# Performance work log

Hardware: AMD Instinct MI355X
Metric: run time of the kernel (lower is better)

Reference implementation:

```python
import jax, jax.numpy as jnp
import numpy as np

D_QK = 32  # out_channels // 8


def conv1x1(x, w, b):
    # x: [B,C,H,W], w: [O,C], b: [O] -> [B,O,H,W]
    return jnp.einsum('bchw,oc->bohw', x, w) + b[None, :, None, None]


def setup_inputs() -> dict:
    key = jax.random.key(0)
    ks = jax.random.split(key, 10)
    B, C, H, W = 4, 256, 64, 64
    in_ch, out_ch, attn_ch = 512, 256, 256
    s_in = 1.0 / np.sqrt(in_ch)
    s_at = 1.0 / np.sqrt(attn_ch)
    return {
        'ef': jax.random.normal(ks[0], (B, C, H, W), jnp.float32),
        'sf': jax.random.normal(ks[1], (B, C, H, W), jnp.float32),
        'Attn': jax.random.normal(ks[2], (B, attn_ch, H, W), jnp.float32),
        'Qw': jax.random.uniform(ks[3], (D_QK, in_ch), jnp.float32, -s_in, s_in),
        'Qb': jax.random.uniform(ks[4], (D_QK,), jnp.float32, -s_in, s_in),
        'Kw': jax.random.uniform(ks[5], (D_QK, attn_ch), jnp.float32, -s_at, s_at),
        'Kb': jax.random.uniform(ks[6], (D_QK,), jnp.float32, -s_at, s_at),
        'Vw': jax.random.uniform(ks[7], (out_ch, in_ch), jnp.float32, -s_in, s_in),
        'Vb': jax.random.uniform(ks[8], (out_ch,), jnp.float32, -s_in, s_in),
        'gamma': jnp.ones((1,), jnp.float32) * 0.25,
    }


def reference(ef, sf, Attn, Qw, Qb, Kw, Kb, Vw, Vb, gamma):
    B, C, H, W = ef.shape
    N = H * W
    x = jnp.concatenate((ef, sf), axis=1)  # [B, 2C, H, W]
    q = conv1x1(x, Qw, Qb).reshape(B, D_QK, N)         # [B, d, N]
    k = conv1x1(Attn, Kw, Kb).reshape(B, D_QK, N)      # [B, d, N]
    # scores[b, m, n] = sum_d q[b, d, m] * k[b, d, n]  (no 1/sqrt(d) scale)
    scores = jnp.einsum('bdm,bdn->bmn', q, k)
    attn = jax.nn.softmax(scores, axis=-1)             # [B, N, N]
    v = conv1x1(x, Vw, Vb).reshape(B, C, N)            # [B, C, N]
    # out[b, c, m] = sum_n v[b, c, n] * attn[b, m, n]
    out = jnp.einsum('bcn,bmn->bcm', v, attn).reshape(B, C, H, W)
    return gamma[0] * out + ef
```

## Files before the change

kernel.cpp:

```cpp
#include <hip/hip_runtime.h>
#include <hip/hip_bf16.h>

typedef short bf16x8 __attribute__((ext_vector_type(8)));
typedef float f32x4 __attribute__((ext_vector_type(4)));

#define MFMA16(a, b, c) __builtin_amdgcn_mfma_f32_16x16x32_bf16(a, b, c, 0, 0, 0)

#define NB 4
#define NC 256
#define NSP 4096
#define LOG2E 1.4426950408889634f

__device__ __forceinline__ unsigned short f2bf(float f) {
    return (unsigned short)((__float_as_uint(f) + 0x8000u) >> 16);
}
__device__ __forceinline__ unsigned pk2bf(float hi, float lo) {
    return __builtin_amdgcn_perm(__float_as_uint(hi) + 0x8000u,
                                 __float_as_uint(lo) + 0x8000u, 0x07060302u);
}

__global__ __launch_bounds__(256) void prep_w(
    const float* __restrict__ Qw, const float* __restrict__ Kw,
    const float* __restrict__ Vw,
    unsigned short* __restrict__ Qwbf, unsigned short* __restrict__ Kwbf,
    unsigned short* __restrict__ Vwbf)
{
    int i = blockIdx.x * 256 + threadIdx.x;
    {
        const float4* vs = (const float4*)(Vw + (size_t)i * 8);
        float4 a = vs[0], c = vs[1];
        int4 st;
        st.x = (int)pk2bf(a.y, a.x); st.y = (int)pk2bf(a.w, a.z);
        st.z = (int)pk2bf(c.y, c.x); st.w = (int)pk2bf(c.w, c.z);
        *(int4*)(Vwbf + (size_t)i * 8) = st;
    }
    if (i < 2048) {
        const float4* qs = (const float4*)(Qw + (size_t)i * 8);
        float4 a = qs[0], c = qs[1];
        int4 st;
        st.x = (int)pk2bf(a.y, a.x); st.y = (int)pk2bf(a.w, a.z);
        st.z = (int)pk2bf(c.y, c.x); st.w = (int)pk2bf(c.w, c.z);
        *(int4*)(Qwbf + (size_t)i * 8) = st;
    }
    if (i < 1024) {
        const float4* ks = (const float4*)(Kw + (size_t)i * 8);
        float4 a = ks[0], c = ks[1];
        int4 st;
        st.x = (int)pk2bf(a.y, a.x); st.y = (int)pk2bf(a.w, a.z);
        st.z = (int)pk2bf(c.y, c.x); st.w = (int)pk2bf(c.w, c.z);
        *(int4*)(Kwbf + (size_t)i * 8) = st;
    }
}

__global__ __launch_bounds__(256) void proj_qv(
    const float* __restrict__ ef, const float* __restrict__ sf,
    const unsigned short* __restrict__ Qwbf, const float* __restrict__ Qb,
    const unsigned short* __restrict__ Vwbf, const float* __restrict__ Vb,
    unsigned short* __restrict__ qws, unsigned short* __restrict__ vws)
{
    __shared__ __align__(16) unsigned short xt[32][72];

    int t = threadIdx.x;
    int w = t >> 6, lane = t & 63, quad = lane >> 4, l15 = lane & 15;
    int mt = blockIdx.x, b = blockIdx.y, m0 = mt * 32;
    int ci = t & 63, sm = t >> 6;
    int mi = w >> 1, oh = w & 1;

    f32x4 zero = {0.f, 0.f, 0.f, 0.f};
    f32x4 acc[2][4];
#pragma unroll
    for (int m = 0; m < 2; ++m)
#pragma unroll
        for (int ot = 0; ot < 4; ++ot) acc[m][ot] = zero;
    f32x4 qacc = zero;

    const float* s0p = ef + ((size_t)(b * NC) + ci) * NSP + m0 + sm * 8;
    float4 x0 = *(const float4*)s0p;
    float4 x1 = *(const float4*)(s0p + 4);

    for (int c = 0; c < 8; ++c) {
        float4 n0 = x0, n1 = x1;
        if (c < 7) {
            int cn = c + 1;
            const float* sn = (cn < 4 ? ef : sf) +
                              ((size_t)(b * NC) + (cn & 3) * 64 + ci) * NSP + m0 + sm * 8;
            n0 = *(const float4*)sn;
            n1 = *(const float4*)(sn + 4);
        }
        __syncthreads();
        unsigned short* xd = &xt[sm * 8][ci];
        xd[0]   = f2bf(x0.x); xd[72]  = f2bf(x0.y);
        xd[144] = f2bf(x0.z); xd[216] = f2bf(x0.w);
        xd[288] = f2bf(x1.x); xd[360] = f2bf(x1.y);
        xd[432] = f2bf(x1.z); xd[504] = f2bf(x1.w);
        __syncthreads();
        int ci0 = c * 64;
#pragma unroll
        for (int ks = 0; ks < 2; ++ks) {
            bf16x8 a0 = *(const bf16x8*)&xt[l15][ks * 32 + quad * 8];
            bf16x8 a1 = *(const bf16x8*)&xt[16 + l15][ks * 32 + quad * 8];
            bf16x8 bq = *(const bf16x8*)(Qwbf + (size_t)(oh * 16 + l15) * 512 + ci0 + ks * 32 + quad * 8);
            qacc = MFMA16(mi ? a1 : a0, bq, qacc);
#pragma unroll
            for (int ot = 0; ot < 4; ++ot) {
                bf16x8 bv = *(const bf16x8*)(Vwbf + (size_t)(w * 64 + ot * 16 + l15) * 512 + ci0 + ks * 32 + quad * 8);
                acc[0][ot] = MFMA16(a0, bv, acc[0][ot]);
                acc[1][ot] = MFMA16(a1, bv, acc[1][ot]);
            }
        }
        x0 = n0; x1 = n1;
    }

#pragma unroll
    for (int ot = 0; ot < 4; ++ot) {
        int ch = w * 64 + ot * 16 + l15;
        float bias = Vb[ch];
        unsigned* vp = (unsigned*)(vws + ((size_t)((b * 128 + mt) * 256 + ch)) * 32);
#pragma unroll
        for (int r = 0; r < 4; ++r)
            vp[quad * 4 + r] = pk2bf(acc[1][ot][r] + bias, acc[0][ot][r] + bias);
    }

    {
        int o = oh * 16 + l15;
        float bb = Qb[o];
#pragma unroll
        for (int r = 0; r < 4; ++r) {
            int m = m0 + mi * 16 + quad * 4 + r;
            qws[((size_t)(b * NSP) + m) * 32 + o] = f2bf((qacc[r] + bb) * LOG2E);
        }
    }
}

__global__ __launch_bounds__(256) void proj_k(
    const float* __restrict__ attn,
    const unsigned short* __restrict__ Kwbf, const float* __restrict__ Kb,
    unsigned short* __restrict__ kws)
{
    __shared__ __align__(16) unsigned short xt[32][72];

    int t = threadIdx.x;
    int w = t >> 6, lane = t & 63, quad = lane >> 4, l15 = lane & 15;
    int mt = blockIdx.x, b = blockIdx.y, m0 = mt * 32;
    int ci = t & 63, sm = t >> 6;
    int mi = w >> 1, oh = w & 1;

    f32x4 acc = {0.f, 0.f, 0.f, 0.f};

    const float* s0p = attn + ((size_t)(b * NC) + ci) * NSP + m0 + sm * 8;
    float4 x0 = *(const float4*)s0p;
    float4 x1 = *(const float4*)(s0p + 4);

    for (int c = 0; c < 4; ++c) {
        float4 n0 = x0, n1 = x1;
        if (c < 3) {
            const float* sn = attn + ((size_t)(b * NC) + (c + 1) * 64 + ci) * NSP + m0 + sm * 8;
            n0 = *(const float4*)sn;
            n1 = *(const float4*)(sn + 4);
        }
        __syncthreads();
        unsigned short* xd = &xt[sm * 8][ci];
        xd[0]   = f2bf(x0.x); xd[72]  = f2bf(x0.y);
        xd[144] = f2bf(x0.z); xd[216] = f2bf(x0.w);
        xd[288] = f2bf(x1.x); xd[360] = f2bf(x1.y);
        xd[432] = f2bf(x1.z); xd[504] = f2bf(x1.w);
        __syncthreads();
        int ci0 = c * 64;
#pragma unroll
        for (int ks = 0; ks < 2; ++ks) {
            bf16x8 a  = *(const bf16x8*)&xt[mi * 16 + l15][ks * 32 + quad * 8];
            bf16x8 bk = *(const bf16x8*)(Kwbf + (size_t)(oh * 16 + l15) * 256 + ci0 + ks * 32 + quad * 8);
            acc = MFMA16(a, bk, acc);
        }
        x0 = n0; x1 = n1;
    }

    int o = oh * 16 + l15;
    float bb = Kb[o];
#pragma unroll
    for (int r = 0; r < 4; ++r) {
        int m = m0 + mi * 16 + quad * 4 + r;
        kws[((size_t)(b * NSP) + m) * 32 + o] = f2bf(acc[r] + bb);
    }
}


#define ATT_ITER(IT, VCUR, VNXT)                                              \
    {                                                                         \
        int buf = (IT) & 1;                                                   \
        f32x4 s0 = MFMA16(qf, kf[0], zero);                                   \
        f32x4 s1 = MFMA16(qf, kf[1], zero);                                   \
        f32x4 s2 = MFMA16(qf, kf[2], zero);                                   \
        f32x4 s3 = MFMA16(qf, kf[3], zero);                                   \
        float e0[4], e1[4], e2[4], e3[4];                                     \
        _Pragma("unroll")                                                     \
        for (int r = 0; r < 4; ++r) {                                         \
            e0[r] = __builtin_amdgcn_exp2f(s0[r]);                            \
            e1[r] = __builtin_amdgcn_exp2f(s1[r]);                            \
            e2[r] = __builtin_amdgcn_exp2f(s2[r]);                            \
            e3[r] = __builtin_amdgcn_exp2f(s3[r]);                            \
        }                                                                     \
        lp0 += (e0[0] + e1[0]) + (e2[0] + e3[0]);                             \
        lp1 += (e0[1] + e1[1]) + (e2[1] + e3[1]);                             \
        lp2 += (e0[2] + e1[2]) + (e2[2] + e3[2]);                             \
        lp3 += (e0[3] + e1[3]) + (e2[3] + e3[3]);                             \
        unsigned short* pd = &Plds[g][buf][(w * 16 + quad * 4) * 72 + 2 * l15]; \
        _Pragma("unroll")                                                     \
        for (int r = 0; r < 4; ++r) {                                         \
            *(unsigned*)(pd + r * 72)      = pk2bf(e1[r], e0[r]);             \
            *(unsigned*)(pd + r * 72 + 32) = pk2bf(e3[r], e2[r]);             \
        }                                                                     \
        int itn = (IT) + 1 < 32 ? (IT) + 1 : 31;                              \
        int ttn = tt0 + 2 * itn;                                              \
        _Pragma("unroll")                                                     \
        for (int j = 0; j < 4; ++j)                                           \
            kf[j] = *(const bf16x8*)(kbase + (size_t)((ttn + (j >> 1)) * 32 + (j & 1) * 16 + l15) * 32 + quad * 8); \
        _Pragma("unroll")                                                     \
        for (int h = 0; h < 2; ++h)                                           \
            _Pragma("unroll")                                                 \
            for (int cc = 0; cc < 4; ++cc)                                    \
                VNXT[h][cc] = *(const bf16x8*)(vbase + (size_t)(ttn + h) * 8192 + (w * 64 + cc * 16 + l15) * 32 + quad * 8); \
        __syncthreads();                                                      \
        _Pragma("unroll")                                                     \
        for (int h = 0; h < 2; ++h) {                                         \
            bf16x8 pa0 = *(const bf16x8*)&Plds[g][buf][(0  + l15) * 72 + h * 32 + quad * 8]; \
            bf16x8 pa1 = *(const bf16x8*)&Plds[g][buf][(16 + l15) * 72 + h * 32 + quad * 8]; \
            bf16x8 pa2 = *(const bf16x8*)&Plds[g][buf][(32 + l15) * 72 + h * 32 + quad * 8]; \
            bf16x8 pa3 = *(const bf16x8*)&Plds[g][buf][(48 + l15) * 72 + h * 32 + quad * 8]; \
            _Pragma("unroll")                                                 \
            for (int cc = 0; cc < 4; ++cc) {                                  \
                acc[0][cc] = MFMA16(pa0, VCUR[h][cc], acc[0][cc]);            \
                acc[1][cc] = MFMA16(pa1, VCUR[h][cc], acc[1][cc]);            \
                acc[2][cc] = MFMA16(pa2, VCUR[h][cc], acc[2][cc]);            \
                acc[3][cc] = MFMA16(pa3, VCUR[h][cc], acc[3][cc]);            \
            }                                                                 \
        }                                                                     \
    }

__global__ __launch_bounds__(512, 2) void attention(
    const unsigned short* __restrict__ qws, const unsigned short* __restrict__ kws,
    const unsigned short* __restrict__ vws, const float* __restrict__ ef,
    const float* __restrict__ gamma, float* __restrict__ out)
{
    __shared__ unsigned short Plds[2][2][64 * 72];
    __shared__ float mrg[256][68];
    __shared__ float denl[2][64];

    int t = threadIdx.x;
    int g = t >> 8, tl = t & 255;
    int w = tl >> 6, lane = tl & 63, quad = lane >> 4, l15 = lane & 15;
    int b = blockIdx.x >> 6, m0 = (blockIdx.x & 63) << 6;

    const unsigned short* kbase = kws + (size_t)(b * NSP) * 32;
    const unsigned short* vbase = vws + (size_t)(b * 128) * 8192;

    bf16x8 qf = *(const bf16x8*)(qws + ((size_t)(b * NSP) + m0 + w * 16 + l15) * 32 + quad * 8);

    f32x4 zero = {0.f, 0.f, 0.f, 0.f};
    f32x4 acc[4][4];
#pragma unroll
    for (int i = 0; i < 4; ++i)
#pragma unroll
        for (int j = 0; j < 4; ++j) acc[i][j] = zero;
    float lp0 = 0.f, lp1 = 0.f, lp2 = 0.f, lp3 = 0.f;

    int tt0 = g * 64;
    bf16x8 kf[4];
#pragma unroll
    for (int j = 0; j < 4; ++j)
        kf[j] = *(const bf16x8*)(kbase + (size_t)((tt0 + (j >> 1)) * 32 + (j & 1) * 16 + l15) * 32 + quad * 8);
    bf16x8 vfA[2][4], vfB[2][4];
#pragma unroll
    for (int h = 0; h < 2; ++h)
#pragma unroll
        for (int cc = 0; cc < 4; ++cc)
            vfA[h][cc] = *(const bf16x8*)(vbase + (size_t)(tt0 + h) * 8192 + (w * 64 + cc * 16 + l15) * 32 + quad * 8);

    for (int it2 = 0; it2 < 16; ++it2) {
        ATT_ITER(2 * it2,     vfA, vfB);
        ATT_ITER(2 * it2 + 1, vfB, vfA);
    }

    lp0 += __shfl_xor(lp0, 1); lp0 += __shfl_xor(lp0, 2); lp0 += __shfl_xor(lp0, 4); lp0 += __shfl_xor(lp0, 8);
    lp1 += __shfl_xor(lp1, 1); lp1 += __shfl_xor(lp1, 2); lp1 += __shfl_xor(lp1, 4); lp1 += __shfl_xor(lp1, 8);
    lp2 += __shfl_xor(lp2, 1); lp2 += __shfl_xor(lp2, 2); lp2 += __shfl_xor(lp2, 4); lp2 += __shfl_xor(lp2, 8);
    lp3 += __shfl_xor(lp3, 1); lp3 += __shfl_xor(lp3, 2); lp3 += __shfl_xor(lp3, 4); lp3 += __shfl_xor(lp3, 8);
    if (l15 == 0) {
        int base = w * 16 + quad * 4;
        denl[g][base + 0] = lp0; denl[g][base + 1] = lp1;
        denl[g][base + 2] = lp2; denl[g][base + 3] = lp3;
    }
    if (g == 1) {
#pragma unroll
        for (int qc = 0; qc < 4; ++qc)
#pragma unroll
            for (int cc = 0; cc < 4; ++cc)
                *(f32x4*)&mrg[w * 64 + cc * 16 + l15][qc * 16 + quad * 4] = acc[qc][cc];
    }
    __syncthreads();

    if (g == 0) {
        float gam = gamma[0];
#pragma unroll
        for (int qc = 0; qc < 4; ++qc) {
            int qb = qc * 16 + quad * 4;
            float4 d0 = *(const float4*)&denl[0][qb];
            float4 d1 = *(const float4*)&denl[1][qb];
            float r0 = gam / (d0.x + d1.x), r1 = gam / (d0.y + d1.y);
            float r2 = gam / (d0.z + d1.z), r3 = gam / (d0.w + d1.w);
#pragma unroll
            for (int cc = 0; cc < 4; ++cc) {
                int ch = w * 64 + cc * 16 + l15;
                f32x4 part = *(const f32x4*)&mrg[ch][qb];
                size_t off = ((size_t)(b * NC + ch)) * NSP + m0 + qb;
                float4 e = *(const float4*)(ef + off);
                float4 o;
                o.x = (acc[qc][cc][0] + part[0]) * r0 + e.x;
                o.y = (acc[qc][cc][1] + part[1]) * r1 + e.y;
                o.z = (acc[qc][cc][2] + part[2]) * r2 + e.z;
                o.w = (acc[qc][cc][3] + part[3]) * r3 + e.w;
                *(float4*)(out + off) = o;
            }
        }
    }
}

extern "C" void kernel_launch(void* const* d_in, const int* in_sizes, int n_in,
                              void* d_out, int out_size, void* d_ws, size_t ws_size,
                              hipStream_t stream) {
    const float* ef    = (const float*)d_in[0];
    const float* sf    = (const float*)d_in[1];
    const float* attn  = (const float*)d_in[2];
    const float* Qw    = (const float*)d_in[3];
    const float* Qb    = (const float*)d_in[4];
    const float* Kw    = (const float*)d_in[5];
    const float* Kb    = (const float*)d_in[6];
    const float* Vw    = (const float*)d_in[7];
    const float* Vb    = (const float*)d_in[8];
    const float* gamma = (const float*)d_in[9];
    float* out = (float*)d_out;

    unsigned short* qws  = (unsigned short*)d_ws;
    unsigned short* kws  = qws + (size_t)4 * 4096 * 32;
    unsigned short* vws  = kws + (size_t)4 * 4096 * 32;
    unsigned short* Qwbf = vws + (size_t)4 * 128 * 256 * 32;
    unsigned short* Kwbf = Qwbf + 32 * 512;
    unsigned short* Vwbf = Kwbf + 32 * 256;

    hipLaunchKernelGGL(prep_w, dim3(64), dim3(256), 0, stream,
                       Qw, Kw, Vw, Qwbf, Kwbf, Vwbf);
    hipLaunchKernelGGL(proj_qv, dim3(128, 4), dim3(256), 0, stream,
                       ef, sf, Qwbf, Qb, Vwbf, Vb, qws, vws);
    hipLaunchKernelGGL(proj_k, dim3(128, 4), dim3(256), 0, stream,
                       attn, Kwbf, Kb, kws);
    hipLaunchKernelGGL(attention, dim3(256), dim3(512), 0, stream,
                       qws, kws, vws, ef, gamma, out);
}
```

Measured before the change: 178.6 us.

## Software-pipeline attention: overlap next tile's scores and exp with PV MFMAs

The attention loop is restructured so that the QK scores and exp2 for tile i+1 are computed and written to the alternate P buffer while the PV MFMAs for tile i run. A prologue handles the first tile and the final iteration skips the lookahead. K is now loaded two tiles ahead. The aim is to hide exp and LDS-store latency behind matrix work, at the cost of more live registers. Separately, the projection kernels now load two channel rows per thread and store packed bf16 pairs as 32-bit LDS writes, which halves the number of shared-memory stores.

```diff
diff --git a/kernel.cpp b/kernel.cpp
--- a/kernel.cpp
+++ b/kernel.cpp
@@ -63,7 +63,7 @@
     int t = threadIdx.x;
     int w = t >> 6, lane = t & 63, quad = lane >> 4, l15 = lane & 15;
     int mt = blockIdx.x, b = blockIdx.y, m0 = mt * 32;
-    int ci = t & 63, sm = t >> 6;
+    int u = t & 7, v = t >> 3;
     int mi = w >> 1, oh = w & 1;
 
     f32x4 zero = {0.f, 0.f, 0.f, 0.f};
@@ -74,25 +74,25 @@
         for (int ot = 0; ot < 4; ++ot) acc[m][ot] = zero;
     f32x4 qacc = zero;
 
-    const float* s0p = ef + ((size_t)(b * NC) + ci) * NSP + m0 + sm * 8;
-    float4 x0 = *(const float4*)s0p;
-    float4 x1 = *(const float4*)(s0p + 4);
+    const float* s0p = ef + ((size_t)(b * NC) + 2 * v) * NSP + m0 + u * 4;
+    float4 xA = *(const float4*)s0p;
+    float4 xB = *(const float4*)(s0p + NSP);
 
     for (int c = 0; c < 8; ++c) {
-        float4 n0 = x0, n1 = x1;
+        float4 nA = xA, nB = xB;
         if (c < 7) {
             int cn = c + 1;
             const float* sn = (cn < 4 ? ef : sf) +
-                              ((size_t)(b * NC) + (cn & 3) * 64 + ci) * NSP + m0 + sm * 8;
-            n0 = *(const float4*)sn;
-            n1 = *(const float4*)(sn + 4);
+                              ((size_t)(b * NC) + (cn & 3) * 64 + 2 * v) * NSP + m0 + u * 4;
+            nA = *(const float4*)sn;
+            nB = *(const float4*)(sn + NSP);
         }
         __syncthreads();
-        unsigned short* xd = &xt[sm * 8][ci];
-        xd[0]   = f2bf(x0.x); xd[72]  = f2bf(x0.y);
-        xd[144] = f2bf(x0.z); xd[216] = f2bf(x0.w);
-        xd[288] = f2bf(x1.x); xd[360] = f2bf(x1.y);
-        xd[432] = f2bf(x1.z); xd[504] = f2bf(x1.w);
+        unsigned* xw = (unsigned*)&xt[u * 4][2 * v];
+        xw[0]   = pk2bf(xB.x, xA.x);
+        xw[36]  = pk2bf(xB.y, xA.y);
+        xw[72]  = pk2bf(xB.z, xA.z);
+        xw[108] = pk2bf(xB.w, xA.w);
         __syncthreads();
         int ci0 = c * 64;
 #pragma unroll
@@ -108,7 +108,7 @@
                 acc[1][ot] = MFMA16(a1, bv, acc[1][ot]);
             }
         }
-        x0 = n0; x1 = n1;
+        xA = nA; xB = nB;
     }
 
 #pragma unroll
@@ -142,28 +142,28 @@
     int t = threadIdx.x;
     int w = t >> 6, lane = t & 63, quad = lane >> 4, l15 = lane & 15;
     int mt = blockIdx.x, b = blockIdx.y, m0 = mt * 32;
-    int ci = t & 63, sm = t >> 6;
+    int u = t & 7, v = t >> 3;
     int mi = w >> 1, oh = w & 1;
 
     f32x4 acc = {0.f, 0.f, 0.f, 0.f};
 
-    const float* s0p = attn + ((size_t)(b * NC) + ci) * NSP + m0 + sm * 8;
-    float4 x0 = *(const float4*)s0p;
-    float4 x1 = *(const float4*)(s0p + 4);
+    const float* s0p = attn + ((size_t)(b * NC) + 2 * v) * NSP + m0 + u * 4;
+    float4 xA = *(const float4*)s0p;
+    float4 xB = *(const float4*)(s0p + NSP);
 
     for (int c = 0; c < 4; ++c) {
-        float4 n0 = x0, n1 = x1;
+        float4 nA = xA, nB = xB;
         if (c < 3) {
-            const float* sn = attn + ((size_t)(b * NC) + (c + 1) * 64 + ci) * NSP + m0 + sm * 8;
-            n0 = *(const float4*)sn;
-            n1 = *(const float4*)(sn + 4);
+            const float* sn = attn + ((size_t)(b * NC) + (c + 1) * 64 + 2 * v) * NSP + m0 + u * 4;
+            nA = *(const float4*)sn;
+            nB = *(const float4*)(sn + NSP);
         }
         __syncthreads();
-        unsigned short* xd = &xt[sm * 8][ci];
-        xd[0]   = f2bf(x0.x); xd[72]  = f2bf(x0.y);
-        xd[144] = f2bf(x0.z); xd[216] = f2bf(x0.w);
-        xd[288] = f2bf(x1.x); xd[360] = f2bf(x1.y);
-        xd[432] = f2bf(x1.z); xd[504] = f2bf(x1.w);
+        unsigned* xw = (unsigned*)&xt[u * 4][2 * v];
+        xw[0]   = pk2bf(xB.x, xA.x);
+        xw[36]  = pk2bf(xB.y, xA.y);
+        xw[72]  = pk2bf(xB.z, xA.z);
+        xw[108] = pk2bf(xB.w, xA.w);
         __syncthreads();
         int ci0 = c * 64;
 #pragma unroll
@@ -172,7 +172,7 @@
             bf16x8 bk = *(const bf16x8*)(Kwbf + (size_t)(oh * 16 + l15) * 256 + ci0 + ks * 32 + quad * 8);
             acc = MFMA16(a, bk, acc);
         }
-        x0 = n0; x1 = n1;
+        xA = nA; xB = nB;
     }
 
     int o = oh * 16 + l15;
@@ -184,43 +184,30 @@
     }
 }
 
-
-#define ATT_ITER(IT, VCUR, VNXT)                                              \
+#define ATT_PIPE(IT, VCUR, VNXT, DONEXT)                                      \
     {                                                                         \
         int buf = (IT) & 1;                                                   \
-        f32x4 s0 = MFMA16(qf, kf[0], zero);                                   \
-        f32x4 s1 = MFMA16(qf, kf[1], zero);                                   \
-        f32x4 s2 = MFMA16(qf, kf[2], zero);                                   \
-        f32x4 s3 = MFMA16(qf, kf[3], zero);                                   \
-        float e0[4], e1[4], e2[4], e3[4];                                     \
-        _Pragma("unroll")                                                     \
-        for (int r = 0; r < 4; ++r) {                                         \
-            e0[r] = __builtin_amdgcn_exp2f(s0[r]);                            \
-            e1[r] = __builtin_amdgcn_exp2f(s1[r]);                            \
-            e2[r] = __builtin_amdgcn_exp2f(s2[r]);                            \
-            e3[r] = __builtin_amdgcn_exp2f(s3[r]);                            \
+        __syncthreads();     \
+        f32x4 s0, s1, s2, s3;                                                 \
+        if (DONEXT) {                                                         \
+            s0 = MFMA16(qf, kf[0], zero);                                     \
+            s1 = MFMA16(qf, kf[1], zero);                                     \
+            s2 = MFMA16(qf, kf[2], zero);                                     \
+            s3 = MFMA16(qf, kf[3], zero);                                     \
         }                                                                     \
-        lp0 += (e0[0] + e1[0]) + (e2[0] + e3[0]);                             \
-        lp1 += (e0[1] + e1[1]) + (e2[1] + e3[1]);                             \
-        lp2 += (e0[2] + e1[2]) + (e2[2] + e3[2]);                             \
-        lp3 += (e0[3] + e1[3]) + (e2[3] + e3[3]);                             \
-        unsigned short* pd = &Plds[g][buf][(w * 16 + quad * 4) * 72 + 2 * l15]; \
-        _Pragma("unroll")                                                     \
-        for (int r = 0; r < 4; ++r) {                                         \
-            *(unsigned*)(pd + r * 72)      = pk2bf(e1[r], e0[r]);             \
-            *(unsigned*)(pd + r * 72 + 32) = pk2bf(e3[r], e2[r]);             \
+        if (DONEXT) {                                                         \
+            int tk = (IT) + 2 < 32 ? (IT) + 2 : 31;                           \
+            int tv = (IT) + 1 < 32 ? (IT) + 1 : 31;                           \
+            int ttk = tt0 + 2 * tk, ttv = tt0 + 2 * tv;                       \
+            _Pragma("unroll")                                                 \
+            for (int j = 0; j < 4; ++j)                                       \
+                kf[j] = *(const bf16x8*)(kbase + (size_t)((ttk + (j >> 1)) * 32 + (j & 1) * 16 + l15) * 32 + quad * 8); \
+            _Pragma("unroll")                                                 \
+            for (int h = 0; h < 2; ++h)                                       \
+                _Pragma("unroll")                                             \
+                for (int cc = 0; cc < 4; ++cc)                                \
+                    VNXT[h][cc] = *(const bf16x8*)(vbase + (size_t)(ttv + h) * 8192 + (w * 64 + cc * 16 + l15) * 32 + quad * 8); \
         }                                                                     \
-        int itn = (IT) + 1 < 32 ? (IT) + 1 : 31;                              \
-        int ttn = tt0 + 2 * itn;                                              \
-        _Pragma("unroll")                                                     \
-        for (int j = 0; j < 4; ++j)                                           \
-            kf[j] = *(const bf16x8*)(kbase + (size_t)((ttn + (j >> 1)) * 32 + (j & 1) * 16 + l15) * 32 + quad * 8); \
-        _Pragma("unroll")                                                     \
-        for (int h = 0; h < 2; ++h)                                           \
-            _Pragma("unroll")                                                 \
-            for (int cc = 0; cc < 4; ++cc)                                    \
-                VNXT[h][cc] = *(const bf16x8*)(vbase + (size_t)(ttn + h) * 8192 + (w * 64 + cc * 16 + l15) * 32 + quad * 8); \
-        __syncthreads();                                                      \
         _Pragma("unroll")                                                     \
         for (int h = 0; h < 2; ++h) {                                         \
             bf16x8 pa0 = *(const bf16x8*)&Plds[g][buf][(0  + l15) * 72 + h * 32 + quad * 8]; \
@@ -233,6 +220,26 @@
                 acc[1][cc] = MFMA16(pa1, VCUR[h][cc], acc[1][cc]);            \
                 acc[2][cc] = MFMA16(pa2, VCUR[h][cc], acc[2][cc]);            \
                 acc[3][cc] = MFMA16(pa3, VCUR[h][cc], acc[3][cc]);            \
+            }                                                                 \
+        }                                                                     \
+        if (DONEXT) {                                                         \
+            float e0[4], e1[4], e2[4], e3[4];                                 \
+            _Pragma("unroll")                                                 \
+            for (int r = 0; r < 4; ++r) {                                     \
+                e0[r] = __builtin_amdgcn_exp2f(s0[r]);                        \
+                e1[r] = __builtin_amdgcn_exp2f(s1[r]);                        \
+                e2[r] = __builtin_amdgcn_exp2f(s2[r]);                        \
+                e3[r] = __builtin_amdgcn_exp2f(s3[r]);                        \
+            }                                                                 \
+            lp0 += (e0[0] + e1[0]) + (e2[0] + e3[0]);                         \
+            lp1 += (e0[1] + e1[1]) + (e2[1] + e3[1]);                         \
+            lp2 += (e0[2] + e1[2]) + (e2[2] + e3[2]);                         \
+            lp3 += (e0[3] + e1[3]) + (e2[3] + e3[3]);                         \
+            unsigned short* pd = &Plds[g][buf ^ 1][(w * 16 + quad * 4) * 72 + 2 * l15]; \
+            _Pragma("unroll")                                                 \
+            for (int r = 0; r < 4; ++r) {                                     \
+                *(unsigned*)(pd + r * 72)      = pk2bf(e1[r], e0[r]);         \
+                *(unsigned*)(pd + r * 72 + 32) = pk2bf(e3[r], e2[r]);         \
             }                                                                 \
         }                                                                     \
     }
@@ -269,6 +276,34 @@
 #pragma unroll
     for (int j = 0; j < 4; ++j)
         kf[j] = *(const bf16x8*)(kbase + (size_t)((tt0 + (j >> 1)) * 32 + (j & 1) * 16 + l15) * 32 + quad * 8);
+
+    {
+        f32x4 s0 = MFMA16(qf, kf[0], zero);
+        f32x4 s1 = MFMA16(qf, kf[1], zero);
+        f32x4 s2 = MFMA16(qf, kf[2], zero);
+        f32x4 s3 = MFMA16(qf, kf[3], zero);
+        float e0[4], e1[4], e2[4], e3[4];
+#pragma unroll
+        for (int r = 0; r < 4; ++r) {
+            e0[r] = __builtin_amdgcn_exp2f(s0[r]);
+            e1[r] = __builtin_amdgcn_exp2f(s1[r]);
+            e2[r] = __builtin_amdgcn_exp2f(s2[r]);
+            e3[r] = __builtin_amdgcn_exp2f(s3[r]);
+        }
+        lp0 += (e0[0] + e1[0]) + (e2[0] + e3[0]);
+        lp1 += (e0[1] + e1[1]) + (e2[1] + e3[1]);
+        lp2 += (e0[2] + e1[2]) + (e2[2] + e3[2]);
+        lp3 += (e0[3] + e1[3]) + (e2[3] + e3[3]);
+        unsigned short* pd = &Plds[g][0][(w * 16 + quad * 4) * 72 + 2 * l15];
+#pragma unroll
+        for (int r = 0; r < 4; ++r) {
+            *(unsigned*)(pd + r * 72)      = pk2bf(e1[r], e0[r]);
+            *(unsigned*)(pd + r * 72 + 32) = pk2bf(e3[r], e2[r]);
+        }
+    }
+#pragma unroll
+    for (int j = 0; j < 4; ++j)
+        kf[j] = *(const bf16x8*)(kbase + (size_t)((tt0 + 2 + (j >> 1)) * 32 + (j & 1) * 16 + l15) * 32 + quad * 8);
     bf16x8 vfA[2][4], vfB[2][4];
 #pragma unroll
     for (int h = 0; h < 2; ++h)
@@ -276,10 +311,12 @@
         for (int cc = 0; cc < 4; ++cc)
             vfA[h][cc] = *(const bf16x8*)(vbase + (size_t)(tt0 + h) * 8192 + (w * 64 + cc * 16 + l15) * 32 + quad * 8);
 
-    for (int it2 = 0; it2 < 16; ++it2) {
-        ATT_ITER(2 * it2,     vfA, vfB);
-        ATT_ITER(2 * it2 + 1, vfB, vfA);
-    }
+    for (int it2 = 0; it2 < 15; ++it2) {
+        ATT_PIPE(2 * it2,     vfA, vfB, 1);
+        ATT_PIPE(2 * it2 + 1, vfB, vfA, 1);
+    }
+    ATT_PIPE(30, vfA, vfB, 1);
+    ATT_PIPE(31, vfB, vfA, 0);
 
     lp0 += __shfl_xor(lp0, 1); lp0 += __shfl_xor(lp0, 2); lp0 += __shfl_xor(lp0, 4); lp0 += __shfl_xor(lp0, 8);
     lp1 += __shfl_xor(lp1, 1); lp1 += __shfl_xor(lp1, 2); lp1 += __shfl_xor(lp1, 4); lp1 += __shfl_xor(lp1, 8);
```

New measurement: 174.5 us. 1.02x faster.

## Hoist all projection input loads upfront and double-buffer packed LDS tiles

Applied to the files above, without the earlier changes.

Both projection kernels now issue every global float4 load for their input channels at kernel start instead of prefetching one chunk per iteration. This puts many loads in flight at once to hide HBM latency. Each thread now covers two adjacent channels and writes packed 32-bit bf16 pairs to LDS rather than scattered 16-bit stores. The LDS tile is double-buffered, which leaves one barrier per iteration, and launch bounds request two blocks per CU. The cost is much higher register pressure from holding all input chunks at once, which may limit occupancy or cause spills.

```diff
diff --git a/kernel.cpp b/kernel.cpp
--- a/kernel.cpp
+++ b/kernel.cpp
@@ -52,19 +52,28 @@
     }
 }
 
-__global__ __launch_bounds__(256) void proj_qv(
+__global__ __launch_bounds__(256, 2) void proj_qv(
     const float* __restrict__ ef, const float* __restrict__ sf,
     const unsigned short* __restrict__ Qwbf, const float* __restrict__ Qb,
     const unsigned short* __restrict__ Vwbf, const float* __restrict__ Vb,
     unsigned short* __restrict__ qws, unsigned short* __restrict__ vws)
 {
-    __shared__ __align__(16) unsigned short xt[32][72];
+    __shared__ __align__(16) unsigned short xt[2][32][72];
 
     int t = threadIdx.x;
     int w = t >> 6, lane = t & 63, quad = lane >> 4, l15 = lane & 15;
     int mt = blockIdx.x, b = blockIdx.y, m0 = mt * 32;
-    int ci = t & 63, sm = t >> 6;
+    int u = t & 7, v = t >> 3;
     int mi = w >> 1, oh = w & 1;
+
+    float4 xA[8], xB[8];
+#pragma unroll
+    for (int c = 0; c < 8; ++c) {
+        const float* sp = (c < 4 ? ef : sf) +
+                          ((size_t)(b * NC) + (c & 3) * 64 + 2 * v) * NSP + m0 + u * 4;
+        xA[c] = *(const float4*)sp;
+        xB[c] = *(const float4*)(sp + NSP);
+    }
 
     f32x4 zero = {0.f, 0.f, 0.f, 0.f};
     f32x4 acc[2][4];
@@ -74,31 +83,19 @@
         for (int ot = 0; ot < 4; ++ot) acc[m][ot] = zero;
     f32x4 qacc = zero;
 
-    const float* s0p = ef + ((size_t)(b * NC) + ci) * NSP + m0 + sm * 8;
-    float4 x0 = *(const float4*)s0p;
-    float4 x1 = *(const float4*)(s0p + 4);
-
+#pragma unroll
     for (int c = 0; c < 8; ++c) {
-        float4 n0 = x0, n1 = x1;
-        if (c < 7) {
-            int cn = c + 1;
-            const float* sn = (cn < 4 ? ef : sf) +
-                              ((size_t)(b * NC) + (cn & 3) * 64 + ci) * NSP + m0 + sm * 8;
-            n0 = *(const float4*)sn;
-            n1 = *(const float4*)(sn + 4);
-        }
-        __syncthreads();
-        unsigned short* xd = &xt[sm * 8][ci];
-        xd[0]   = f2bf(x0.x); xd[72]  = f2bf(x0.y);
-        xd[144] = f2bf(x0.z); xd[216] = f2bf(x0.w);
-        xd[288] = f2bf(x1.x); xd[360] = f2bf(x1.y);
-        xd[432] = f2bf(x1.z); xd[504] = f2bf(x1.w);
+        unsigned* xw = (unsigned*)&xt[c & 1][u * 4][2 * v];
+        xw[0]   = pk2bf(xB[c].x, xA[c].x);
+        xw[36]  = pk2bf(xB[c].y, xA[c].y);
+        xw[72]  = pk2bf(xB[c].z, xA[c].z);
+        xw[108] = pk2bf(xB[c].w, xA[c].w);
         __syncthreads();
         int ci0 = c * 64;
 #pragma unroll
         for (int ks = 0; ks < 2; ++ks) {
-            bf16x8 a0 = *(const bf16x8*)&xt[l15][ks * 32 + quad * 8];
-            bf16x8 a1 = *(const bf16x8*)&xt[16 + l15][ks * 32 + quad * 8];
+            bf16x8 a0 = *(const bf16x8*)&xt[c & 1][l15][ks * 32 + quad * 8];
+            bf16x8 a1 = *(const bf16x8*)&xt[c & 1][16 + l15][ks * 32 + quad * 8];
             bf16x8 bq = *(const bf16x8*)(Qwbf + (size_t)(oh * 16 + l15) * 512 + ci0 + ks * 32 + quad * 8);
             qacc = MFMA16(mi ? a1 : a0, bq, qacc);
 #pragma unroll
@@ -108,7 +105,6 @@
                 acc[1][ot] = MFMA16(a1, bv, acc[1][ot]);
             }
         }
-        x0 = n0; x1 = n1;
     }
 
 #pragma unroll
@@ -132,47 +128,44 @@
     }
 }
 
-__global__ __launch_bounds__(256) void proj_k(
+__global__ __launch_bounds__(256, 2) void proj_k(
     const float* __restrict__ attn,
     const unsigned short* __restrict__ Kwbf, const float* __restrict__ Kb,
     unsigned short* __restrict__ kws)
 {
-    __shared__ __align__(16) unsigned short xt[32][72];
+    __shared__ __align__(16) unsigned short xt[2][32][72];
 
     int t = threadIdx.x;
     int w = t >> 6, lane = t & 63, quad = lane >> 4, l15 = lane & 15;
     int mt = blockIdx.x, b = blockIdx.y, m0 = mt * 32;
-    int ci = t & 63, sm = t >> 6;
+    int u = t & 7, v = t >> 3;
     int mi = w >> 1, oh = w & 1;
 
+    float4 xA[4], xB[4];
+#pragma unroll
+    for (int c = 0; c < 4; ++c) {
+        const float* sp = attn + ((size_t)(b * NC) + c * 64 + 2 * v) * NSP + m0 + u * 4;
+        xA[c] = *(const float4*)sp;
+        xB[c] = *(const float4*)(sp + NSP);
+    }
+
     f32x4 acc = {0.f, 0.f, 0.f, 0.f};
 
-    const float* s0p = attn + ((size_t)(b * NC) + ci) * NSP + m0 + sm * 8;
-    float4 x0 = *(const float4*)s0p;
-    float4 x1 = *(const float4*)(s0p + 4);
-
+#pragma unroll
     for (int c = 0; c < 4; ++c) {
-        float4 n0 = x0, n1 = x1;
-        if (c < 3) {
-            const float* sn = attn + ((size_t)(b * NC) + (c + 1) * 64 + ci) * NSP + m0 + sm * 8;
-            n0 = *(const float4*)sn;
-            n1 = *(const float4*)(sn + 4);
-        }
-        __syncthreads();
-        unsigned short* xd = &xt[sm * 8][ci];
-        xd[0]   = f2bf(x0.x); xd[72]  = f2bf(x0.y);
-        xd[144] = f2bf(x0.z); xd[216] = f2bf(x0.w);
-        xd[288] = f2bf(x1.x); xd[360] = f2bf(x1.y);
-        xd[432] = f2bf(x1.z); xd[504] = f2bf(x1.w);
+        unsigned* xw = (unsigned*)&xt[c & 1][u * 4][2 * v];
+        xw[0]   = pk2bf(xB[c].x, xA[c].x);
+        xw[36]  = pk2bf(xB[c].y, xA[c].y);
+        xw[72]  = pk2bf(xB[c].z, xA[c].z);
+        xw[108] = pk2bf(xB[c].w, xA[c].w);
         __syncthreads();
         int ci0 = c * 64;
 #pragma unroll
         for (int ks = 0; ks < 2; ++ks) {
-            bf16x8 a  = *(const bf16x8*)&xt[mi * 16 + l15][ks * 32 + quad * 8];
+            bf16x8 a  = *(const bf16x8*)&xt[c & 1][mi * 16 + l15][ks * 32 + quad * 8];
             bf16x8 bk = *(const bf16x8*)(Kwbf + (size_t)(oh * 16 + l15) * 256 + ci0 + ks * 32 + quad * 8);
             acc = MFMA16(a, bk, acc);
         }
-        x0 = n0; x1 = n1;
     }
 
     int o = oh * 16 + l15;
@@ -183,7 +176,6 @@
         kws[((size_t)(b * NSP) + m) * 32 + o] = f2bf(acc[r] + bb);
     }
 }
-
 
 #define ATT_ITER(IT, VCUR, VNXT)                                              \
     {                                                                         \
```

Result: no change. 179.8 us (+0.7%).
